# Optimization experiments

Measured on AMD Instinct MI355X. Metric: run time of the kernel, lower is better.

Reference implementation:

```python
import jax, jax.numpy as jnp
import numpy as np

BATCH, IN, HID, OUT = 4096, 1024, 2048, 1000
ITERS = 50
LR = 0.001


def setup_inputs() -> dict:
    key = jax.random.key(0)
    k1, k2, k3 = jax.random.split(key, 3)
    x = jax.random.uniform(k1, (BATCH, IN), dtype=jnp.float32)
    # xavier_uniform for W_rec [HID, IN] and W_out [OUT, HID]
    lim_rec = float(np.sqrt(6.0 / (HID + IN)))
    lim_out = float(np.sqrt(6.0 / (OUT + HID)))
    W_rec = jax.random.uniform(k2, (HID, IN), minval=-lim_rec, maxval=lim_rec, dtype=jnp.float32)
    W_out = jax.random.uniform(k3, (OUT, HID), minval=-lim_out, maxval=lim_out, dtype=jnp.float32)
    bias_out = jnp.zeros((OUT,), dtype=jnp.float32)
    bias_gen = jnp.zeros((IN,), dtype=jnp.float32)
    return {"x": x, "W_rec": W_rec, "W_out": W_out, "bias_out": bias_out, "bias_gen": bias_gen}


def reference(x, W_rec, W_out, bias_out, bias_gen):
    batch = x.shape[0]
    h0 = jnp.zeros((batch, HID), dtype=x.dtype)
    y0 = jnp.zeros((batch, OUT), dtype=x.dtype)

    def step(carry, _):
        h, y, total_e = carry
        # generative prediction of input: sigmoid(h @ W_rec + bias_gen) [B, IN]
        x_pred = jax.nn.sigmoid(jnp.matmul(h, W_rec) + bias_gen)
        e_x = x - x_pred
        h = h + LR * jnp.matmul(e_x, W_rec.T)          # [B, HID]
        y_pred = jnp.matmul(h, W_out.T) + bias_out     # [B, OUT]
        e_y = y - y_pred
        y = y + LR * e_y
        energy = jnp.mean(jnp.sum(e_x * e_x, axis=1)) + jnp.mean(jnp.sum(e_y * e_y, axis=1))
        return (h, y, total_e + energy), None

    (h, y, total_energy), _ = jax.lax.scan(step, (h0, y0, jnp.float32(0.0)), None, length=ITERS)
    average_energy = total_energy / ITERS
    return y, average_energy
```

## Files before the change

kernel.cpp:

```cpp
#include <hip/hip_runtime.h>
#include <hip/hip_bf16.h>
#include <cstdint>

typedef __bf16 bf16_t;
typedef __bf16 bf16x4 __attribute__((ext_vector_type(4)));
typedef __bf16 bf16x8 __attribute__((ext_vector_type(8)));
typedef float f32x4 __attribute__((ext_vector_type(4)));

#define BATCH 4096
#define DIN   1024
#define HID   2048
#define DOUT  1000
#define NITER 50
#define LR    0.001f

#define BM 128
#define BN 128
#define BK 32
#define NBUF 4

#define GLDS(g, l)                                                        \
    __builtin_amdgcn_global_load_lds(                                     \
        (const __attribute__((address_space(1))) void*)(g),               \
        (__attribute__((address_space(3))) void*)(l), 16, 0, 0)

#define WAITVM(N) asm volatile("s_waitcnt vmcnt(" #N ")" ::: "memory")
#define BAR()     __builtin_amdgcn_s_barrier()
#define SCHEDB()  __builtin_amdgcn_sched_barrier(0)

template <int MODE>
__global__ __launch_bounds__(512) void pc_gemm(
    const bf16_t* __restrict__ Aex, bf16_t* __restrict__ wrecT,
    bf16_t* __restrict__ woutP, bf16_t* __restrict__ wg,
    bf16_t* __restrict__ wc,
    const bf16_t* __restrict__ xbf, const float* __restrict__ bias_g,
    const float* __restrict__ bias_o,
    bf16_t* __restrict__ exnext, bf16_t* __restrict__ u,
    bf16_t* __restrict__ z, bf16_t* __restrict__ ey,
    float* __restrict__ yout, float* __restrict__ energy)
{
    __shared__ __align__(16) bf16_t sA[NBUF][BM * BK];
    __shared__ __align__(16) bf16_t sB[NBUF][BN * BK];
    __shared__ float red[8];

    const int t    = threadIdx.x;
    const int lane = t & 63;
    const int wave = t >> 6;
    const int wm   = wave >> 2;
    const int wn   = wave & 3;
    const int m0   = blockIdx.x * BM;
    const int lr   = lane & 15;
    const int lkb  = (lane >> 4) * 8;

    int role, n0, K;
    const bf16_t *Aop, *Bop;
    if constexpr (MODE == 3) {
        role = (int)blockIdx.y >= 8; n0 = ((int)blockIdx.y & 7) * BN; K = HID;
        Aop = role ? woutP : wrecT;  Bop = wrecT;
    } else if constexpr (MODE == 2) {
        role = 1; n0 = (int)blockIdx.y * BN; K = DIN;
        Aop = Aex; Bop = wc;
    } else {
        role = (int)blockIdx.y >= 8; n0 = ((int)blockIdx.y & 7) * BN; K = DIN;
        Aop = Aex; Bop = role ? wc : wg;
    }

    f32x4 acc[4][2] = {};

    const int srow = wave * 16 + (lane >> 2);
    const int scol = (lane & 3) * 8;
    const bf16_t* gA = Aop + (int64_t)(m0 + srow) * K + scol;
    const bf16_t* gB = Bop + (int64_t)(n0 + srow) * K + scol;

    auto stage = [&](int tile, int buf) {
        const int64_t ko = (int64_t)tile * BK;
        GLDS(gA + ko, &sA[buf][wave * 512]);
        GLDS(gB + ko, &sB[buf][wave * 512]);
    };

    auto compute = [&](int buf) {
        bf16x8 af[4], bfr[2];
#pragma unroll
        for (int mi = 0; mi < 4; ++mi)
            af[mi] = *reinterpret_cast<const bf16x8*>(
                &sA[buf][(wm * 64 + mi * 16 + lr) * BK + lkb]);
#pragma unroll
        for (int ni = 0; ni < 2; ++ni)
            bfr[ni] = *reinterpret_cast<const bf16x8*>(
                &sB[buf][(wn * 32 + ni * 16 + lr) * BK + lkb]);
#pragma unroll
        for (int mi = 0; mi < 4; ++mi)
#pragma unroll
            for (int ni = 0; ni < 2; ++ni)
                acc[mi][ni] = __builtin_amdgcn_mfma_f32_16x16x32_bf16(
                    af[mi], bfr[ni], acc[mi][ni], 0, 0, 0);
    };

    const int npairs = (K / BK) / 2;
    stage(0, 0); stage(1, 1); stage(2, 2); stage(3, 3);

    for (int p = 0; p < npairs - 2; ++p) {
        const int t0 = 2 * p;
        WAITVM(4);
        BAR();
        SCHEDB();
        compute(t0 & 3);
        compute((t0 + 1) & 3);
        BAR();
        stage(t0 + 4, t0 & 3);
        stage(t0 + 5, (t0 + 1) & 3);
    }
    {
        const int t0 = 2 * npairs - 4;
        WAITVM(4); BAR(); SCHEDB();
        compute(t0 & 3); compute((t0 + 1) & 3);
    }
    {
        const int t0 = 2 * npairs - 2;
        WAITVM(0); BAR(); SCHEDB();
        compute(t0 & 3); compute((t0 + 1) & 3);
    }

    float esum = 0.0f;
    const int prow = (lane >> 4) * 4;
#pragma unroll
    for (int mi = 0; mi < 4; ++mi) {
#pragma unroll
        for (int ni = 0; ni < 2; ++ni) {
            const int col = n0 + wn * 32 + ni * 16 + lr;
#pragma unroll
            for (int j = 0; j < 4; ++j) {
                const int row = m0 + wm * 64 + mi * 16 + prow + j;
                const float v = acc[mi][ni][j];
                if constexpr (MODE == 3) {
                    bf16_t* cout = role ? wc : wg;
                    cout[(int64_t)row * 1024 + col] = (bf16_t)v;
                } else {
                    if (role == 0) {
                        const int64_t idx = (int64_t)row * DIN + col;
                        const float D  = LR * v;
                        const float un =
                            (MODE == 1 ? bias_g[col] : (float)u[idx]) + D;
                        u[idx] = (bf16_t)un;
                        const float xp = 1.0f / (1.0f + __expf(-un));
                        const float e  = (float)xbf[idx] - xp;
                        exnext[idx] = (bf16_t)e;
                        esum += e * e;
                    } else if (col < DOUT) {
                        const int64_t idx = (int64_t)row * 1024 + col;
                        const float D  = LR * v;
                        const float zn =
                            (MODE == 1 ? bias_o[col] : (float)z[idx]) + D;
                        const float eyn = (MODE == 1)
                            ? -zn
                            : (1.0f + LR) * (float)ey[idx] - D;
                        if constexpr (MODE == 2) {
                            yout[(int64_t)row * DOUT + col] =
                                (1.0f + LR) * eyn + zn;
                        } else {
                            z[idx]  = (bf16_t)zn;
                            ey[idx] = (bf16_t)eyn;
                        }
                        esum += eyn * eyn;
                    }
                }
            }
        }
    }
    if constexpr (MODE != 3) {
#pragma unroll
        for (int off = 32; off; off >>= 1) esum += __shfl_down(esum, off, 64);
        if (lane == 0) red[wave] = esum;
        __syncthreads();
        if (t == 0) {
            float s = 0.0f;
#pragma unroll
            for (int w = 0; w < 8; ++w) s += red[w];
            atomicAdd(energy, s);
        }
    }
}

__global__ void conv_wrec(const float* __restrict__ W, bf16_t* __restrict__ WbT)
{
    __shared__ float tile[32][33];
    const int tx = threadIdx.x & 31;
    const int ty = threadIdx.x >> 5;
    const int c0 = blockIdx.x * 32;
    const int r0 = blockIdx.y * 32;
#pragma unroll
    for (int rr = ty; rr < 32; rr += 8)
        tile[rr][tx] = W[(int64_t)(r0 + rr) * DIN + c0 + tx];
    __syncthreads();
#pragma unroll
    for (int rr = ty; rr < 32; rr += 8)
        WbT[(int64_t)(c0 + rr) * HID + r0 + tx] = (bf16_t)tile[tx][rr];
}

__global__ void conv_wout(const float* __restrict__ W, bf16_t* __restrict__ Wb)
{
    const int i = blockIdx.x * 256 + threadIdx.x;
    const int r = i >> 11;
    const int c = i & 2047;
    Wb[i] = (r < DOUT) ? (bf16_t)W[(int64_t)r * HID + c] : (bf16_t)0.0f;
}

__global__ void ex0_kernel(const float* __restrict__ x,
                           const float* __restrict__ bias_g,
                           bf16_t* __restrict__ ex, bf16_t* __restrict__ xbf,
                           float* __restrict__ energy)
{
    __shared__ float red[4];
    const int t = threadIdx.x, lane = t & 63, wave = t >> 6;
    const int i = (blockIdx.x * 256 + t) * 4;
    const int c0 = i & (DIN - 1);
    const float4 v = *reinterpret_cast<const float4*>(&x[i]);
    bf16x4 xo = {(bf16_t)v.x, (bf16_t)v.y, (bf16_t)v.z, (bf16_t)v.w};
    *reinterpret_cast<bf16x4*>(&xbf[i]) = xo;
    float e[4];
    const float b0 = bias_g[c0], b1 = bias_g[c0 + 1],
                b2 = bias_g[c0 + 2], b3 = bias_g[c0 + 3];
    e[0] = v.x - 1.0f / (1.0f + __expf(-b0));
    e[1] = v.y - 1.0f / (1.0f + __expf(-b1));
    e[2] = v.z - 1.0f / (1.0f + __expf(-b2));
    e[3] = v.w - 1.0f / (1.0f + __expf(-b3));
    bf16x4 o = {(bf16_t)e[0], (bf16_t)e[1], (bf16_t)e[2], (bf16_t)e[3]};
    *reinterpret_cast<bf16x4*>(&ex[i]) = o;
    float esum = e[0]*e[0] + e[1]*e[1] + e[2]*e[2] + e[3]*e[3];
#pragma unroll
    for (int off = 32; off; off >>= 1) esum += __shfl_down(esum, off, 64);
    if (lane == 0) red[wave] = esum;
    __syncthreads();
    if (t == 0) atomicAdd(energy, red[0] + red[1] + red[2] + red[3]);
}

__global__ void finalize_kernel(const float* __restrict__ energy,
                                float* __restrict__ out)
{
    out[0] = energy[0] * (1.0f / ((float)BATCH * (float)NITER));
}

extern "C" void kernel_launch(void* const* d_in, const int* in_sizes, int n_in,
                              void* d_out, int out_size, void* d_ws, size_t ws_size,
                              hipStream_t stream)
{
    (void)in_sizes; (void)n_in; (void)out_size; (void)ws_size;
    const float* x        = (const float*)d_in[0];
    const float* W_rec    = (const float*)d_in[1];
    const float* W_out    = (const float*)d_in[2];
    const float* bias_out = (const float*)d_in[3];
    const float* bias_gen = (const float*)d_in[4];
    float* y = (float*)d_out;

    char* ws = (char*)d_ws;
    size_t off = 0;
    bf16_t* u     = (bf16_t*)(ws + off);  off += (size_t)BATCH * DIN * 2;
    bf16_t* z     = (bf16_t*)(ws + off);  off += (size_t)BATCH * 1024 * 2;
    bf16_t* exA   = (bf16_t*)(ws + off);  off += (size_t)BATCH * DIN * 2;
    bf16_t* exB   = (bf16_t*)(ws + off);  off += (size_t)BATCH * DIN * 2;
    bf16_t* ey    = (bf16_t*)(ws + off);  off += (size_t)BATCH * 1024 * 2;
    bf16_t* xbf   = (bf16_t*)(ws + off);  off += (size_t)BATCH * DIN * 2;
    bf16_t* wrecT = (bf16_t*)(ws + off);  off += (size_t)DIN * HID * 2;
    bf16_t* woutP = (bf16_t*)(ws + off);  off += (size_t)1024 * HID * 2;
    bf16_t* wg    = (bf16_t*)(ws + off);  off += (size_t)1024 * 1024 * 2;
    bf16_t* wc    = (bf16_t*)(ws + off);  off += (size_t)1024 * 1024 * 2;
    float* energy = (float*)(ws + off);   off += 256;

    hipMemsetAsync(energy, 0, 4, stream);

    conv_wrec<<<dim3(DIN / 32, HID / 32), 256, 0, stream>>>(W_rec, wrecT);
    conv_wout<<<(1024 * HID) / 256, 256, 0, stream>>>(W_out, woutP);
    pc_gemm<3><<<dim3(8, 16), 512, 0, stream>>>(
        nullptr, wrecT, woutP, wg, wc, nullptr, nullptr, nullptr,
        nullptr, nullptr, nullptr, nullptr, nullptr, nullptr);

    ex0_kernel<<<(BATCH * DIN) / 1024, 256, 0, stream>>>(x, bias_gen, exA,
                                                         xbf, energy);

    bf16_t* exbuf[2] = {exA, exB};
    for (int it = 0; it < NITER; ++it) {
        const bf16_t* src = exbuf[it & 1];
        bf16_t* dst = exbuf[(it & 1) ^ 1];
        if (it == 0)
            pc_gemm<1><<<dim3(BATCH / BM, 16), 512, 0, stream>>>(
                src, nullptr, nullptr, wg, wc, xbf, bias_gen, bias_out,
                dst, u, z, ey, nullptr, energy);
        else if (it < NITER - 1)
            pc_gemm<0><<<dim3(BATCH / BM, 16), 512, 0, stream>>>(
                src, nullptr, nullptr, wg, wc, xbf, bias_gen, bias_out,
                dst, u, z, ey, nullptr, energy);
        else
            pc_gemm<2><<<dim3(BATCH / BM, 8), 512, 0, stream>>>(
                src, nullptr, nullptr, wg, wc, xbf, bias_gen, bias_out,
                nullptr, u, z, ey, y, energy);
    }
    finalize_kernel<<<1, 1, 0, stream>>>(energy, y + (size_t)BATCH * DOUT);
}
```

Baseline: 1.853 ms.

## Shrink per-iteration GEMM tiles to 64x128 with 4 waves and split setup kernel

The per-iteration GEMM now uses 64-row tiles, 256 threads (4 waves each owning a 32-column slice), a 3-deep single-tile pipeline, and a flattened 1D grid where consecutive blocks share the same column tile. The one-time weight-product GEMM moves into its own setup_gemm kernel that keeps the old 128x128 configuration. The goal is more blocks (1024 instead of 512) for better CU occupancy and load balance on the 4096x2048 iteration GEMM, plus L2 reuse of B tiles across neighbouring blocks. In exchange, each block reloads B for fewer rows, so global/LDS traffic per FLOP rises.

```diff
diff --git a/kernel.cpp b/kernel.cpp
--- a/kernel.cpp
+++ b/kernel.cpp
@@ -14,10 +14,10 @@
 #define NITER 50
 #define LR    0.001f
 
-#define BM 128
+#define BM 64
 #define BN 128
 #define BK 32
-#define NBUF 4
+#define NBUF 3
 
 #define GLDS(g, l)                                                        \
     __builtin_amdgcn_global_load_lds(                                     \
@@ -29,10 +29,9 @@
 #define SCHEDB()  __builtin_amdgcn_sched_barrier(0)
 
 template <int MODE>
-__global__ __launch_bounds__(512) void pc_gemm(
-    const bf16_t* __restrict__ Aex, bf16_t* __restrict__ wrecT,
-    bf16_t* __restrict__ woutP, bf16_t* __restrict__ wg,
-    bf16_t* __restrict__ wc,
+__global__ __launch_bounds__(256) void pc_gemm(
+    const bf16_t* __restrict__ Aex,
+    const bf16_t* __restrict__ wg, const bf16_t* __restrict__ wc,
     const bf16_t* __restrict__ xbf, const float* __restrict__ bias_g,
     const float* __restrict__ bias_o,
     bf16_t* __restrict__ exnext, bf16_t* __restrict__ u,
@@ -41,43 +40,148 @@
 {
     __shared__ __align__(16) bf16_t sA[NBUF][BM * BK];
     __shared__ __align__(16) bf16_t sB[NBUF][BN * BK];
-    __shared__ float red[8];
+    __shared__ float red[4];
+
+    const int t    = threadIdx.x;
+    const int lane = t & 63;
+    const int wave = t >> 6;
+    const int bid  = blockIdx.x;
+    const int m    = bid & 63;
+    const int sub  = bid >> 6;
+    const int role = (MODE == 2) ? 1 : (sub >> 3);
+    const int n0   = (MODE == 2) ? sub * BN : (sub & 7) * BN;
+    const int m0   = m * BM;
+    const int lr   = lane & 15;
+    const int lkb  = (lane >> 4) * 8;
+    const int prow = (lane >> 4) * 4;
+
+    const bf16_t* Bop = role ? wc : wg;
+
+    const int srow = lane >> 2;
+    const int scol = (lane & 3) * 8;
+    const bf16_t* gA  = Aex + (int64_t)(m0 + wave * 16 + srow) * DIN + scol;
+    const bf16_t* gB0 = Bop + (int64_t)(n0 + wave * 32 + srow) * DIN + scol;
+    const bf16_t* gB1 = gB0 + (int64_t)16 * DIN;
+
+    f32x4 acc[4][2] = {};
+
+    auto stage = [&](int tile, int buf) {
+        const int64_t ko = (int64_t)tile * BK;
+        GLDS(gA  + ko, &sA[buf][wave * 512]);
+        GLDS(gB0 + ko, &sB[buf][wave * 1024]);
+        GLDS(gB1 + ko, &sB[buf][wave * 1024 + 512]);
+    };
+    auto compute = [&](int buf) {
+        bf16x8 af[4], bfr[2];
+#pragma unroll
+        for (int mi = 0; mi < 4; ++mi)
+            af[mi] = *reinterpret_cast<const bf16x8*>(
+                &sA[buf][(mi * 16 + lr) * BK + lkb]);
+#pragma unroll
+        for (int ni = 0; ni < 2; ++ni)
+            bfr[ni] = *reinterpret_cast<const bf16x8*>(
+                &sB[buf][(wave * 32 + ni * 16 + lr) * BK + lkb]);
+#pragma unroll
+        for (int mi = 0; mi < 4; ++mi)
+#pragma unroll
+            for (int ni = 0; ni < 2; ++ni)
+                acc[mi][ni] = __builtin_amdgcn_mfma_f32_16x16x32_bf16(
+                    af[mi], bfr[ni], acc[mi][ni], 0, 0, 0);
+    };
+
+    const int nt = DIN / BK;
+    stage(0, 0); stage(1, 1); stage(2, 2);
+
+    for (int ts = 0; ts < nt - 3; ++ts) {
+        WAITVM(6);
+        BAR();
+        SCHEDB();
+        compute(ts % 3);
+        BAR();
+        stage(ts + 3, ts % 3);
+    }
+    WAITVM(6); BAR(); SCHEDB(); compute((nt - 3) % 3);
+    WAITVM(3); BAR(); SCHEDB(); compute((nt - 2) % 3);
+    WAITVM(0); BAR(); SCHEDB(); compute((nt - 1) % 3);
+
+    float esum = 0.0f;
+#pragma unroll
+    for (int mi = 0; mi < 4; ++mi) {
+#pragma unroll
+        for (int ni = 0; ni < 2; ++ni) {
+            const int col = n0 + wave * 32 + ni * 16 + lr;
+#pragma unroll
+            for (int j = 0; j < 4; ++j) {
+                const int row = m0 + mi * 16 + prow + j;
+                const float v = acc[mi][ni][j];
+                const float D = LR * v;
+                if (role == 0) {
+                    const int64_t idx = (int64_t)row * DIN + col;
+                    const float un =
+                        (MODE == 1 ? bias_g[col] : (float)u[idx]) + D;
+                    u[idx] = (bf16_t)un;
+                    const float xp = 1.0f / (1.0f + __expf(-un));
+                    const float e  = (float)xbf[idx] - xp;
+                    exnext[idx] = (bf16_t)e;
+                    esum += e * e;
+                } else if (col < DOUT) {
+                    const int64_t idx = (int64_t)row * 1024 + col;
+                    const float zn =
+                        (MODE == 1 ? bias_o[col] : (float)z[idx]) + D;
+                    const float eyn = (MODE == 1)
+                        ? -zn
+                        : (1.0f + LR) * (float)ey[idx] - D;
+                    if constexpr (MODE == 2) {
+                        yout[(int64_t)row * DOUT + col] =
+                            (1.0f + LR) * eyn + zn;
+                    } else {
+                        z[idx]  = (bf16_t)zn;
+                        ey[idx] = (bf16_t)eyn;
+                    }
+                    esum += eyn * eyn;
+                }
+            }
+        }
+    }
+#pragma unroll
+    for (int off = 32; off; off >>= 1) esum += __shfl_down(esum, off, 64);
+    if (lane == 0) red[wave] = esum;
+    __syncthreads();
+    if (t == 0)
+        atomicAdd(energy, red[0] + red[1] + red[2] + red[3]);
+}
+
+__global__ __launch_bounds__(512) void setup_gemm(
+    const bf16_t* __restrict__ wrecT, const bf16_t* __restrict__ woutP,
+    bf16_t* __restrict__ wg, bf16_t* __restrict__ wc)
+{
+    __shared__ __align__(16) bf16_t sA[4][128 * BK];
+    __shared__ __align__(16) bf16_t sB[4][128 * BK];
 
     const int t    = threadIdx.x;
     const int lane = t & 63;
     const int wave = t >> 6;
     const int wm   = wave >> 2;
     const int wn   = wave & 3;
-    const int m0   = blockIdx.x * BM;
+    const int m0   = blockIdx.x * 128;
+    const int role = (int)blockIdx.y >= 8;
+    const int n0   = ((int)blockIdx.y & 7) * 128;
     const int lr   = lane & 15;
     const int lkb  = (lane >> 4) * 8;
-
-    int role, n0, K;
-    const bf16_t *Aop, *Bop;
-    if constexpr (MODE == 3) {
-        role = (int)blockIdx.y >= 8; n0 = ((int)blockIdx.y & 7) * BN; K = HID;
-        Aop = role ? woutP : wrecT;  Bop = wrecT;
-    } else if constexpr (MODE == 2) {
-        role = 1; n0 = (int)blockIdx.y * BN; K = DIN;
-        Aop = Aex; Bop = wc;
-    } else {
-        role = (int)blockIdx.y >= 8; n0 = ((int)blockIdx.y & 7) * BN; K = DIN;
-        Aop = Aex; Bop = role ? wc : wg;
-    }
+    const int prow = (lane >> 4) * 4;
 
     f32x4 acc[4][2] = {};
 
     const int srow = wave * 16 + (lane >> 2);
     const int scol = (lane & 3) * 8;
-    const bf16_t* gA = Aop + (int64_t)(m0 + srow) * K + scol;
-    const bf16_t* gB = Bop + (int64_t)(n0 + srow) * K + scol;
+    const bf16_t* gA = (role ? woutP : wrecT) + (int64_t)(m0 + srow) * HID + scol;
+    const bf16_t* gB = wrecT + (int64_t)(n0 + srow) * HID + scol;
 
     auto stage = [&](int tile, int buf) {
         const int64_t ko = (int64_t)tile * BK;
         GLDS(gA + ko, &sA[buf][wave * 512]);
         GLDS(gB + ko, &sB[buf][wave * 512]);
     };
-
     auto compute = [&](int buf) {
         bf16x8 af[4], bfr[2];
 #pragma unroll
@@ -96,19 +200,14 @@
                     af[mi], bfr[ni], acc[mi][ni], 0, 0, 0);
     };
 
-    const int npairs = (K / BK) / 2;
+    const int npairs = (HID / BK) / 2;
     stage(0, 0); stage(1, 1); stage(2, 2); stage(3, 3);
-
     for (int p = 0; p < npairs - 2; ++p) {
         const int t0 = 2 * p;
-        WAITVM(4);
+        WAITVM(4); BAR(); SCHEDB();
+        compute(t0 & 3); compute((t0 + 1) & 3);
         BAR();
-        SCHEDB();
-        compute(t0 & 3);
-        compute((t0 + 1) & 3);
-        BAR();
-        stage(t0 + 4, t0 & 3);
-        stage(t0 + 5, (t0 + 1) & 3);
+        stage(t0 + 4, t0 & 3); stage(t0 + 5, (t0 + 1) & 3);
     }
     {
         const int t0 = 2 * npairs - 4;
@@ -121,64 +220,18 @@
         compute(t0 & 3); compute((t0 + 1) & 3);
     }
 
-    float esum = 0.0f;
-    const int prow = (lane >> 4) * 4;
-#pragma unroll
-    for (int mi = 0; mi < 4; ++mi) {
+    bf16_t* cout = role ? wc : wg;
+#pragma unroll
+    for (int mi = 0; mi < 4; ++mi)
 #pragma unroll
         for (int ni = 0; ni < 2; ++ni) {
             const int col = n0 + wn * 32 + ni * 16 + lr;
 #pragma unroll
             for (int j = 0; j < 4; ++j) {
                 const int row = m0 + wm * 64 + mi * 16 + prow + j;
-                const float v = acc[mi][ni][j];
-                if constexpr (MODE == 3) {
-                    bf16_t* cout = role ? wc : wg;
-                    cout[(int64_t)row * 1024 + col] = (bf16_t)v;
-                } else {
-                    if (role == 0) {
-                        const int64_t idx = (int64_t)row * DIN + col;
-                        const float D  = LR * v;
-                        const float un =
-                            (MODE == 1 ? bias_g[col] : (float)u[idx]) + D;
-                        u[idx] = (bf16_t)un;
-                        const float xp = 1.0f / (1.0f + __expf(-un));
-                        const float e  = (float)xbf[idx] - xp;
-                        exnext[idx] = (bf16_t)e;
-                        esum += e * e;
-                    } else if (col < DOUT) {
-                        const int64_t idx = (int64_t)row * 1024 + col;
-                        const float D  = LR * v;
-                        const float zn =
-                            (MODE == 1 ? bias_o[col] : (float)z[idx]) + D;
-                        const float eyn = (MODE == 1)
-                            ? -zn
-                            : (1.0f + LR) * (float)ey[idx] - D;
-                        if constexpr (MODE == 2) {
-                            yout[(int64_t)row * DOUT + col] =
-                                (1.0f + LR) * eyn + zn;
-                        } else {
-                            z[idx]  = (bf16_t)zn;
-                            ey[idx] = (bf16_t)eyn;
-                        }
-                        esum += eyn * eyn;
-                    }
-                }
+                cout[(int64_t)row * 1024 + col] = (bf16_t)acc[mi][ni][j];
             }
         }
-    }
-    if constexpr (MODE != 3) {
-#pragma unroll
-        for (int off = 32; off; off >>= 1) esum += __shfl_down(esum, off, 64);
-        if (lane == 0) red[wave] = esum;
-        __syncthreads();
-        if (t == 0) {
-            float s = 0.0f;
-#pragma unroll
-            for (int w = 0; w < 8; ++w) s += red[w];
-            atomicAdd(energy, s);
-        }
-    }
 }
 
 __global__ void conv_wrec(const float* __restrict__ W, bf16_t* __restrict__ WbT)
@@ -270,10 +323,7 @@
 
     conv_wrec<<<dim3(DIN / 32, HID / 32), 256, 0, stream>>>(W_rec, wrecT);
     conv_wout<<<(1024 * HID) / 256, 256, 0, stream>>>(W_out, woutP);
-    pc_gemm<3><<<dim3(8, 16), 512, 0, stream>>>(
-        nullptr, wrecT, woutP, wg, wc, nullptr, nullptr, nullptr,
-        nullptr, nullptr, nullptr, nullptr, nullptr, nullptr);
-
+    setup_gemm<<<dim3(8, 16), 512, 0, stream>>>(wrecT, woutP, wg, wc);
     ex0_kernel<<<(BATCH * DIN) / 1024, 256, 0, stream>>>(x, bias_gen, exA,
                                                          xbf, energy);
 
@@ -282,16 +332,16 @@
         const bf16_t* src = exbuf[it & 1];
         bf16_t* dst = exbuf[(it & 1) ^ 1];
         if (it == 0)
-            pc_gemm<1><<<dim3(BATCH / BM, 16), 512, 0, stream>>>(
-                src, nullptr, nullptr, wg, wc, xbf, bias_gen, bias_out,
+            pc_gemm<1><<<dim3(1024), 256, 0, stream>>>(
+                src, wg, wc, xbf, bias_gen, bias_out,
                 dst, u, z, ey, nullptr, energy);
         else if (it < NITER - 1)
-            pc_gemm<0><<<dim3(BATCH / BM, 16), 512, 0, stream>>>(
-                src, nullptr, nullptr, wg, wc, xbf, bias_gen, bias_out,
+            pc_gemm<0><<<dim3(1024), 256, 0, stream>>>(
+                src, wg, wc, xbf, bias_gen, bias_out,
                 dst, u, z, ey, nullptr, energy);
         else
-            pc_gemm<2><<<dim3(BATCH / BM, 8), 512, 0, stream>>>(
-                src, nullptr, nullptr, wg, wc, xbf, bias_gen, bias_out,
+            pc_gemm<2><<<dim3(512), 256, 0, stream>>>(
+                src, wg, wc, xbf, bias_gen, bias_out,
                 nullptr, u, z, ey, y, energy);
     }
     finalize_kernel<<<1, 1, 0, stream>>>(energy, y + (size_t)BATCH * DOUT);
```

New measurement: 2.528 ms. +36.5%, slower.
